# Performance work log

Measured on AMD Instinct MI355X. Metric: run time of the kernel, lower is better.

## Reference

```python
import jax, jax.numpy as jnp
import numpy as np

P = 16          # patch_size
EMBED = 768     # embed_dim
HEAD_DIM = 64   # embed_dim // num_heads
ROPE_BASE = 10000.0


def rope_2d(coords, head_dim, base):
    """Axial 2D RoPE. coords: (N, 2) int -> cos, sin each (N, head_dim).
    head_dim is split evenly over the two axes; within an axis, frequency
    pairs are repeated twice (standard rotate-pairs layout)."""
    dpa = head_dim // 2                                   # dims per axis
    inv_freq = 1.0 / (base ** (jnp.arange(0, dpa, 2, dtype=jnp.float32) / dpa))  # (dpa//2,)
    ang = coords.astype(jnp.float32)[:, :, None] * inv_freq[None, None, :]       # (N, 2, dpa//2)
    ang = jnp.repeat(ang, 2, axis=-1).reshape(coords.shape[0], head_dim)          # (N, head_dim)
    return jnp.cos(ang), jnp.sin(ang)


def setup_inputs() -> dict:
    key = jax.random.key(0)
    k1, k2 = jax.random.split(key, 2)
    B, C, H, W = 32, 3, 512, 512
    images = jax.random.normal(k1, (B, C, H, W), dtype=jnp.float32)
    patch_dim = C * P * P
    W_proj = jax.random.normal(k2, (patch_dim, EMBED), dtype=jnp.float32) * (patch_dim ** -0.5)
    b_proj = jnp.zeros((EMBED,), dtype=jnp.float32)
    return {"images": images, "W_proj": W_proj, "b_proj": b_proj}


def reference(images, W_proj, b_proj):
    B, C, H, W = images.shape
    Hp, Wp = H // P, W // P
    N = B * Hp * Wp
    # patchify: c (hp p1) (wp p2) -> (hp wp) (c p1 p2), packed across batch
    x = images.reshape(B, C, Hp, P, Wp, P).transpose(0, 2, 4, 1, 3, 5).reshape(N, C * P * P)
    tokens = x @ W_proj + b_proj                              # (N, EMBED)
    # per-image patch coordinates (identical grid for every image)
    ys, xs = jnp.meshgrid(jnp.arange(Hp), jnp.arange(Wp), indexing='ij')
    coords = jnp.stack([ys, xs], axis=-1).reshape(Hp * Wp, 2)
    patch_coords = jnp.tile(coords, (B, 1))                    # (N, 2)
    rope_cos, rope_sin = rope_2d(patch_coords, HEAD_DIM, ROPE_BASE)
    cu_seqlens = (jnp.arange(B + 1, dtype=jnp.int32) * (Hp * Wp))
    is_patch = jnp.ones((N,), dtype=bool)
    return tokens, cu_seqlens, patch_coords, rope_cos, rope_sin, is_patch
```

## Files before the change

### kernel.cpp

```cpp
#include <hip/hip_runtime.h>
#include <hip/hip_bf16.h>

typedef unsigned short u16;
typedef unsigned int   u32;
typedef __bf16 bf16x8 __attribute__((ext_vector_type(8)));
typedef float  f32x4  __attribute__((ext_vector_type(4)));

#define N_TOK 32768
constexpr long long OFF_TOKENS = 0;
constexpr long long OFF_CU     = 25165824LL;
constexpr long long OFF_COORDS = 25165857LL;
constexpr long long OFF_COS    = 25231393LL;
constexpr long long OFF_SIN    = 27328545LL;
constexpr long long OFF_ISP    = 29425697LL;

__device__ __forceinline__ void split_bf16(float v, u32& h, u32& l) {
    __hip_bfloat16 bh = __float2bfloat16(v);
    float fh = __bfloat162float(bh);
    __hip_bfloat16 bl = __float2bfloat16(v - fh);
    h = (u32)__builtin_bit_cast(u16, bh);
    l = (u32)__builtin_bit_cast(u16, bl);
}

__global__ __launch_bounds__(256) void prep_w(const float* __restrict__ W,
                                              u16* __restrict__ wt) {
    int idx = blockIdx.x * 256 + threadIdx.x;
    if (idx >= 768 * 768) return;
    int k = idx / 768;
    int n = idx - k * 768;
    u32 h, l;
    split_bf16(W[idx], h, l);
    wt[(size_t)n * 768 + k]          = (u16)h;
    wt[589824 + (size_t)n * 768 + k] = (u16)l;
}

__global__ __launch_bounds__(256) void patch_gemm_mfma(
    const float* __restrict__ img, const u16* __restrict__ wt,
    const float* __restrict__ bias, float* __restrict__ out)
{
    __shared__ __align__(16) char smem[32768];
    char* pAh = smem;
    char* pAl = smem + 8192;
    char* pBh = smem + 16384;
    char* pBl = smem + 24576;

    const int tid = threadIdx.x;
    const int bn  = blockIdx.x;
    const int bm  = blockIdx.y;

    const int lane = tid & 63;
    const int wid  = tid >> 6;
    const int wm   = (wid >> 1) << 6;
    const int wn   = (wid & 1) << 6;
    const int lr   = lane & 15;
    const int lg   = lane >> 4;

    const int am  = tid & 127;
    const int alq = tid >> 7;
    const int m   = bm * 128 + am;
    const int bb  = m >> 10;
    const int hp  = (m & 1023) >> 5;
    const int wq  = m & 31;
    const float* abase = img + (size_t)bb * 786432 + (size_t)hp * 8192 + wq * 16;
    const int a_wb = am * 64 + ((alq ^ ((am >> 3) & 1)) << 5);

    const int bnl = tid >> 1;
    const int blq = tid & 1;
    const u16* wbh = wt + (size_t)(bn * 128 + bnl) * 768 + blq * 16;
    const u16* wbl = wbh + 589824;
    const int b_wb = bnl * 64 + ((blq ^ ((bnl >> 3) & 1)) << 5);

    const int swz  = (lr >> 3) & 1;
    const int a_rd = lr * 64 + (((lg >> 1) ^ swz) << 5) + ((lg & 1) << 4);

    f32x4 acc[4][4];
    #pragma unroll
    for (int i = 0; i < 4; i++)
        #pragma unroll
        for (int j = 0; j < 4; j++) acc[i][j] = {0.f, 0.f, 0.f, 0.f};

    #pragma unroll 1
    for (int kt = 0; kt < 24; ++kt) {
        const float* ap = abase + (kt >> 3) * 262144 + ((kt & 7) * 2 + alq) * 512;
        float4 a0 = *(const float4*)(ap);
        float4 a1 = *(const float4*)(ap + 4);
        float4 a2 = *(const float4*)(ap + 8);
        float4 a3 = *(const float4*)(ap + 12);
        const u16* ph = wbh + kt * 32;
        uint4 wh0 = *(const uint4*)(ph);
        uint4 wh1 = *(const uint4*)(ph + 8);
        const u16* pl = wbl + kt * 32;
        uint4 wl0 = *(const uint4*)(pl);
        uint4 wl1 = *(const uint4*)(pl + 8);

        __syncthreads();

        u32 h0,l0,h1,l1,h2,l2,h3,l3;
        uint4 H, L;
        split_bf16(a0.x,h0,l0); split_bf16(a0.y,h1,l1);
        split_bf16(a0.z,h2,l2); split_bf16(a0.w,h3,l3);
        H.x = h0 | (h1 << 16); L.x = l0 | (l1 << 16);
        H.y = h2 | (h3 << 16); L.y = l2 | (l3 << 16);
        split_bf16(a1.x,h0,l0); split_bf16(a1.y,h1,l1);
        split_bf16(a1.z,h2,l2); split_bf16(a1.w,h3,l3);
        H.z = h0 | (h1 << 16); L.z = l0 | (l1 << 16);
        H.w = h2 | (h3 << 16); L.w = l2 | (l3 << 16);
        *(uint4*)(pAh + a_wb) = H;
        *(uint4*)(pAl + a_wb) = L;
        split_bf16(a2.x,h0,l0); split_bf16(a2.y,h1,l1);
        split_bf16(a2.z,h2,l2); split_bf16(a2.w,h3,l3);
        H.x = h0 | (h1 << 16); L.x = l0 | (l1 << 16);
        H.y = h2 | (h3 << 16); L.y = l2 | (l3 << 16);
        split_bf16(a3.x,h0,l0); split_bf16(a3.y,h1,l1);
        split_bf16(a3.z,h2,l2); split_bf16(a3.w,h3,l3);
        H.z = h0 | (h1 << 16); L.z = l0 | (l1 << 16);
        H.w = h2 | (h3 << 16); L.w = l2 | (l3 << 16);
        *(uint4*)(pAh + a_wb + 16) = H;
        *(uint4*)(pAl + a_wb + 16) = L;

        *(uint4*)(pBh + b_wb)      = wh0;
        *(uint4*)(pBh + b_wb + 16) = wh1;
        *(uint4*)(pBl + b_wb)      = wl0;
        *(uint4*)(pBl + b_wb + 16) = wl1;

        __syncthreads();

        bf16x8 ah[4], al[4], bh4[4], bl4[4];
        #pragma unroll
        for (int i = 0; i < 4; i++) {
            const int off = (wm + i * 16) * 64 + a_rd;
            ah[i] = *(const bf16x8*)(pAh + off);
            al[i] = *(const bf16x8*)(pAl + off);
        }
        #pragma unroll
        for (int j = 0; j < 4; j++) {
            const int off = (wn + j * 16) * 64 + a_rd;
            bh4[j] = *(const bf16x8*)(pBh + off);
            bl4[j] = *(const bf16x8*)(pBl + off);
        }

        #pragma unroll
        for (int i = 0; i < 4; i++)
            #pragma unroll
            for (int j = 0; j < 4; j++) {
                acc[i][j] = __builtin_amdgcn_mfma_f32_16x16x32_bf16(ah[i], bh4[j], acc[i][j], 0, 0, 0);
                acc[i][j] = __builtin_amdgcn_mfma_f32_16x16x32_bf16(ah[i], bl4[j], acc[i][j], 0, 0, 0);
                acc[i][j] = __builtin_amdgcn_mfma_f32_16x16x32_bf16(al[i], bh4[j], acc[i][j], 0, 0, 0);
            }
    }

    float bv[4];
    #pragma unroll
    for (int j = 0; j < 4; j++) bv[j] = bias[bn * 128 + wn + j * 16 + lr];
    #pragma unroll
    for (int i = 0; i < 4; i++) {
        const int rb = bm * 128 + wm + i * 16 + lg * 4;
        #pragma unroll
        for (int j = 0; j < 4; j++) {
            const int cg = bn * 128 + wn + j * 16 + lr;
            #pragma unroll
            for (int r = 0; r < 4; r++)
                out[OFF_TOKENS + (size_t)(rb + r) * 768 + cg] = acc[i][j][r] + bv[j];
        }
    }
}

__global__ __launch_bounds__(256) void aux_kernel(float* __restrict__ out)
{
    const int idx = blockIdx.x * 256 + threadIdx.x;
    if (idx >= N_TOK * 32) return;
    const int n  = idx >> 5;
    const int jd = idx & 31;

    const int hp = (n & 1023) >> 5;
    const int wp = n & 31;

    const int coord = (jd < 16) ? hp : wp;
    const int j = jd & 15;
    const float freq = exp2f(-(float)j * 0.8304820237218406f);
    float s, c;
    sincosf((float)coord * freq, &s, &c);

    const long long off = (long long)n * 64 + jd * 2;
    *(float2*)(out + OFF_COS + off) = make_float2(c, c);
    *(float2*)(out + OFF_SIN + off) = make_float2(s, s);

    if (jd == 0) {
        out[OFF_COORDS + 2 * (long long)n]     = (float)hp;
        out[OFF_COORDS + 2 * (long long)n + 1] = (float)wp;
        out[OFF_ISP + n] = 1.0f;
    }
    if (jd == 1 && n < 33) {
        out[OFF_CU + n] = (float)(n * 1024);
    }
}

extern "C" void kernel_launch(void* const* d_in, const int* in_sizes, int n_in,
                              void* d_out, int out_size, void* d_ws, size_t ws_size,
                              hipStream_t stream) {
    const float* img  = (const float*)d_in[0];
    const float* W    = (const float*)d_in[1];
    const float* bias = (const float*)d_in[2];
    float* out = (float*)d_out;
    u16* wt = (u16*)d_ws;

    prep_w<<<2304, 256, 0, stream>>>(W, wt);

    dim3 ggrid(6, 256);
    patch_gemm_mfma<<<ggrid, 256, 0, stream>>>(img, wt, bias, out);

    const int aux_elems = N_TOK * 32;
    aux_kernel<<<(aux_elems + 255) / 256, 256, 0, stream>>>(out);
}
```

Baseline: 314.8 us.

## Drop activation low-half split, prefetch next tile, vectorize weight prep

Activations are now rounded to a single bf16 instead of a hi/lo pair, which removes one of the three MFMAs per tile pair plus the A-low LDS buffer and its stores and loads. Global loads for the next k-tile are issued before the second barrier so they overlap the MFMA work of the current tile. The weight prep kernel is rewritten so each thread converts eight consecutive k values and writes packed 16-byte stores. Precision drops because the activation rounding error is no longer compensated, which may exceed the tolerance.

```diff
diff --git a/kernel.cpp b/kernel.cpp
--- a/kernel.cpp
+++ b/kernel.cpp
@@ -14,35 +14,46 @@
 constexpr long long OFF_SIN    = 27328545LL;
 constexpr long long OFF_ISP    = 29425697LL;
 
-__device__ __forceinline__ void split_bf16(float v, u32& h, u32& l) {
+__device__ __forceinline__ void split_bf16(float v, u16& h, u16& l) {
     __hip_bfloat16 bh = __float2bfloat16(v);
     float fh = __bfloat162float(bh);
     __hip_bfloat16 bl = __float2bfloat16(v - fh);
-    h = (u32)__builtin_bit_cast(u16, bh);
-    l = (u32)__builtin_bit_cast(u16, bl);
-}
-
-__global__ __launch_bounds__(256) void prep_w(const float* __restrict__ W,
+    h = __builtin_bit_cast(u16, bh);
+    l = __builtin_bit_cast(u16, bl);
+}
+
+__device__ __forceinline__ u32 pk2(float lo, float hi) {
+    u32 a = (u32)__builtin_bit_cast(u16, __float2bfloat16(lo));
+    u32 b = (u32)__builtin_bit_cast(u16, __float2bfloat16(hi));
+    return a | (b << 16);
+}
+
+__global__ __launch_bounds__(128) void prep_w(const float* __restrict__ W,
                                               u16* __restrict__ wt) {
-    int idx = blockIdx.x * 256 + threadIdx.x;
-    if (idx >= 768 * 768) return;
-    int k = idx / 768;
-    int n = idx - k * 768;
-    u32 h, l;
-    split_bf16(W[idx], h, l);
-    wt[(size_t)n * 768 + k]          = (u16)h;
-    wt[589824 + (size_t)n * 768 + k] = (u16)l;
+    const int n  = blockIdx.x;
+    const int kg = threadIdx.x;
+    if (kg >= 96) return;
+    u16 h[8], l[8];
+    #pragma unroll
+    for (int r = 0; r < 8; r++)
+        split_bf16(W[(size_t)(kg * 8 + r) * 768 + n], h[r], l[r]);
+    uint4 H, L;
+    H.x = (u32)h[0] | ((u32)h[1] << 16); H.y = (u32)h[2] | ((u32)h[3] << 16);
+    H.z = (u32)h[4] | ((u32)h[5] << 16); H.w = (u32)h[6] | ((u32)h[7] << 16);
+    L.x = (u32)l[0] | ((u32)l[1] << 16); L.y = (u32)l[2] | ((u32)l[3] << 16);
+    L.z = (u32)l[4] | ((u32)l[5] << 16); L.w = (u32)l[6] | ((u32)l[7] << 16);
+    *(uint4*)&wt[(size_t)n * 768 + kg * 8]          = H;
+    *(uint4*)&wt[589824 + (size_t)n * 768 + kg * 8] = L;
 }
 
 __global__ __launch_bounds__(256) void patch_gemm_mfma(
     const float* __restrict__ img, const u16* __restrict__ wt,
     const float* __restrict__ bias, float* __restrict__ out)
 {
-    __shared__ __align__(16) char smem[32768];
+    __shared__ __align__(16) char smem[24576];
     char* pAh = smem;
-    char* pAl = smem + 8192;
-    char* pBh = smem + 16384;
-    char* pBl = smem + 24576;
+    char* pBh = smem + 8192;
+    char* pBl = smem + 16384;
 
     const int tid = threadIdx.x;
     const int bn  = blockIdx.x;
@@ -79,59 +90,45 @@
         #pragma unroll
         for (int j = 0; j < 4; j++) acc[i][j] = {0.f, 0.f, 0.f, 0.f};
 
+    float4 a0, a1, a2, a3;
+    uint4 wh0, wh1, wl0, wl1;
+
+#define LOAD_T(KT)                                                          \
+    {   const float* ap = abase + ((KT) >> 3) * 262144 +                    \
+                          (((KT) & 7) * 2 + alq) * 512;                     \
+        a0 = *(const float4*)(ap);      a1 = *(const float4*)(ap + 4);      \
+        a2 = *(const float4*)(ap + 8);  a3 = *(const float4*)(ap + 12);     \
+        const u16* ph = wbh + (KT) * 32;                                    \
+        wh0 = *(const uint4*)(ph);      wh1 = *(const uint4*)(ph + 8);      \
+        const u16* pl = wbl + (KT) * 32;                                    \
+        wl0 = *(const uint4*)(pl);      wl1 = *(const uint4*)(pl + 8); }
+
+    LOAD_T(0);
+
     #pragma unroll 1
     for (int kt = 0; kt < 24; ++kt) {
-        const float* ap = abase + (kt >> 3) * 262144 + ((kt & 7) * 2 + alq) * 512;
-        float4 a0 = *(const float4*)(ap);
-        float4 a1 = *(const float4*)(ap + 4);
-        float4 a2 = *(const float4*)(ap + 8);
-        float4 a3 = *(const float4*)(ap + 12);
-        const u16* ph = wbh + kt * 32;
-        uint4 wh0 = *(const uint4*)(ph);
-        uint4 wh1 = *(const uint4*)(ph + 8);
-        const u16* pl = wbl + kt * 32;
-        uint4 wl0 = *(const uint4*)(pl);
-        uint4 wl1 = *(const uint4*)(pl + 8);
-
         __syncthreads();
 
-        u32 h0,l0,h1,l1,h2,l2,h3,l3;
-        uint4 H, L;
-        split_bf16(a0.x,h0,l0); split_bf16(a0.y,h1,l1);
-        split_bf16(a0.z,h2,l2); split_bf16(a0.w,h3,l3);
-        H.x = h0 | (h1 << 16); L.x = l0 | (l1 << 16);
-        H.y = h2 | (h3 << 16); L.y = l2 | (l3 << 16);
-        split_bf16(a1.x,h0,l0); split_bf16(a1.y,h1,l1);
-        split_bf16(a1.z,h2,l2); split_bf16(a1.w,h3,l3);
-        H.z = h0 | (h1 << 16); L.z = l0 | (l1 << 16);
-        H.w = h2 | (h3 << 16); L.w = l2 | (l3 << 16);
+        uint4 H;
+        H.x = pk2(a0.x, a0.y); H.y = pk2(a0.z, a0.w);
+        H.z = pk2(a1.x, a1.y); H.w = pk2(a1.z, a1.w);
         *(uint4*)(pAh + a_wb) = H;
-        *(uint4*)(pAl + a_wb) = L;
-        split_bf16(a2.x,h0,l0); split_bf16(a2.y,h1,l1);
-        split_bf16(a2.z,h2,l2); split_bf16(a2.w,h3,l3);
-        H.x = h0 | (h1 << 16); L.x = l0 | (l1 << 16);
-        H.y = h2 | (h3 << 16); L.y = l2 | (l3 << 16);
-        split_bf16(a3.x,h0,l0); split_bf16(a3.y,h1,l1);
-        split_bf16(a3.z,h2,l2); split_bf16(a3.w,h3,l3);
-        H.z = h0 | (h1 << 16); L.z = l0 | (l1 << 16);
-        H.w = h2 | (h3 << 16); L.w = l2 | (l3 << 16);
+        H.x = pk2(a2.x, a2.y); H.y = pk2(a2.z, a2.w);
+        H.z = pk2(a3.x, a3.y); H.w = pk2(a3.z, a3.w);
         *(uint4*)(pAh + a_wb + 16) = H;
-        *(uint4*)(pAl + a_wb + 16) = L;
-
         *(uint4*)(pBh + b_wb)      = wh0;
         *(uint4*)(pBh + b_wb + 16) = wh1;
         *(uint4*)(pBl + b_wb)      = wl0;
         *(uint4*)(pBl + b_wb + 16) = wl1;
 
+        if (kt < 23) LOAD_T(kt + 1);
+
         __syncthreads();
 
-        bf16x8 ah[4], al[4], bh4[4], bl4[4];
-        #pragma unroll
-        for (int i = 0; i < 4; i++) {
-            const int off = (wm + i * 16) * 64 + a_rd;
-            ah[i] = *(const bf16x8*)(pAh + off);
-            al[i] = *(const bf16x8*)(pAl + off);
-        }
+        bf16x8 ah[4], bh4[4], bl4[4];
+        #pragma unroll
+        for (int i = 0; i < 4; i++)
+            ah[i] = *(const bf16x8*)(pAh + (wm + i * 16) * 64 + a_rd);
         #pragma unroll
         for (int j = 0; j < 4; j++) {
             const int off = (wn + j * 16) * 64 + a_rd;
@@ -145,9 +142,9 @@
             for (int j = 0; j < 4; j++) {
                 acc[i][j] = __builtin_amdgcn_mfma_f32_16x16x32_bf16(ah[i], bh4[j], acc[i][j], 0, 0, 0);
                 acc[i][j] = __builtin_amdgcn_mfma_f32_16x16x32_bf16(ah[i], bl4[j], acc[i][j], 0, 0, 0);
-                acc[i][j] = __builtin_amdgcn_mfma_f32_16x16x32_bf16(al[i], bh4[j], acc[i][j], 0, 0, 0);
             }
     }
+#undef LOAD_T
 
     float bv[4];
     #pragma unroll
@@ -204,7 +201,7 @@
     float* out = (float*)d_out;
     u16* wt = (u16*)d_ws;
 
-    prep_w<<<2304, 256, 0, stream>>>(W, wt);
+    prep_w<<<768, 128, 0, stream>>>(W, wt);
 
     dim3 ggrid(6, 256);
     patch_gemm_mfma<<<ggrid, 256, 0, stream>>>(img, wt, bias, out);
```

Result: faster. 289.8 us (-7.9%).
